# Kernel optimization log

Hardware: AMD Instinct MI355X
Metric: run time of the kernel (lower is better)

Reference implementation:

```python
import jax, jax.numpy as jnp
import numpy as np
import math

N_LEVELS = 16
F = 2
LOG2_T = 19
T = 1 << LOG2_T  # 524288 hashmap rows
BASE, FINEST = 16, 512
# b computed in float32 like torch.exp((log(512)-log(16))/15)
B_GROWTH = float(np.exp((np.log(np.float32(FINEST)) - np.log(np.float32(BASE))) / np.float32(N_LEVELS - 1)))
RES = [math.floor(BASE * B_GROWTH ** i) for i in range(N_LEVELS)]
SIZES = [(r + 1) ** 3 if r ** 3 < T else T for r in RES]
OFFS = np.concatenate([[0], np.cumsum(SIZES)]).tolist()
TOTAL_ROWS = OFFS[-1]  # 5269629
# corner order (i,j,k) for i,j,k in {0,1}, i outermost -> matches torch grid_offset
CORNER_OFF = np.array([[i, j, k] for i in (0, 1) for j in (0, 1) for k in (0, 1)], dtype=np.int32)
PRIMES = np.array([1, 2654435761, 805459861], dtype=np.uint32)
N_POINTS = 1048576


def setup_inputs() -> dict:
    key = jax.random.key(0)
    k1, k2 = jax.random.split(key)
    x = jax.random.uniform(k1, (N_POINTS, 3), dtype=jnp.float32, minval=-1.0, maxval=1.0)
    # nn.init.uniform_(-1e-4, 1e-4) on every level's embedding table
    tables = jax.random.uniform(k2, (TOTAL_ROWS, F), dtype=jnp.float32, minval=-1e-4, maxval=1e-4)
    return {"x": x, "tables": tables}


def _level_embed(x, table, res):
    # x: (B,3) in [-1,1]; table: (rows,F); res: python int (static)
    xc = jnp.clip(x, -1.0, 1.0)
    grid = jnp.float32(2.0 / res)  # (box_max-box_min)/resolution
    bl = jnp.floor((xc + 1.0) / grid).astype(jnp.int32)  # (B,3) bottom-left voxel
    vmin = bl.astype(x.dtype) * grid - 1.0               # voxel_min_vertex
    # original uses unclamped x for interpolation weights
    w = (x - vmin) / grid                                # (B,3)
    corners = bl[:, None, :] + jnp.asarray(CORNER_OFF)   # (B,8,3)
    if res ** 3 < T:
        # one-to-one hash: i*res^2 + j*res + k
        idx = corners[..., 0] * (res * res) + corners[..., 1] * res + corners[..., 2]
    else:
        # spatial hash with uint32 wraparound multiplication (matches torch int32 wrap)
        c = corners.astype(jnp.uint32)
        h = (c[..., 0] * PRIMES[0]) ^ (c[..., 1] * PRIMES[1]) ^ (c[..., 2] * PRIMES[2])
        idx = (h & jnp.uint32(T - 1)).astype(jnp.int32)
    e = table[idx]  # (B,8,F) gather
    wx, wy, wz = w[:, 0:1], w[:, 1:2], w[:, 2:3]
    c00 = e[:, 0] * (1 - wx) + e[:, 4] * wx
    c01 = e[:, 1] * (1 - wx) + e[:, 5] * wx
    c10 = e[:, 2] * (1 - wx) + e[:, 6] * wx
    c11 = e[:, 3] * (1 - wx) + e[:, 7] * wx
    c0 = c00 * (1 - wy) + c10 * wy
    c1 = c01 * (1 - wy) + c11 * wy
    return c0 * (1 - wz) + c1 * wz  # (B,F)


def reference(x, tables):
    outs = []
    for i in range(N_LEVELS):
        tab = jax.lax.slice_in_dim(tables, OFFS[i], OFFS[i + 1], axis=0)
        outs.append(_level_embed(x, tab, RES[i]))
    return jnp.concatenate(outs, axis=-1)  # (B, n_levels*F) = (B,32)
```

## Files before the change

kernel.cpp:

```cpp
#include <hip/hip_runtime.h>

#define NLVL 16
#define T_MASK ((1u << 19) - 1)
#define NBIN 32768

typedef float v2f __attribute__((ext_vector_type(2)));
typedef float v4f __attribute__((ext_vector_type(4)));

__constant__ int c_res[NLVL] = {16, 20, 25, 32, 40, 50, 64, 80,
                                101, 128, 161, 203, 256, 322, 406, 512};
__constant__ int c_off[NLVL] = {0, 4913, 14174, 31750, 67687, 136608, 269259, 543884,
                                1075325, 1599613, 2123901, 2648189, 3172477, 3696765, 4221053, 4745341};
__constant__ float c_grid[NLVL] = {
    (float)(2.0 / 16.0),  (float)(2.0 / 20.0),  (float)(2.0 / 25.0),  (float)(2.0 / 32.0),
    (float)(2.0 / 40.0),  (float)(2.0 / 50.0),  (float)(2.0 / 64.0),  (float)(2.0 / 80.0),
    (float)(2.0 / 101.0), (float)(2.0 / 128.0), (float)(2.0 / 161.0), (float)(2.0 / 203.0),
    (float)(2.0 / 256.0), (float)(2.0 / 322.0), (float)(2.0 / 406.0), (float)(2.0 / 512.0)};

constexpr int kRes[8] = {16, 20, 25, 32, 40, 50, 64, 80};
constexpr int kOff[8] = {0, 4913, 14174, 31750, 67687, 136608, 269259, 543884};
constexpr float kGrid[8] = {
    (float)(2.0 / 16.0), (float)(2.0 / 20.0), (float)(2.0 / 25.0), (float)(2.0 / 32.0),
    (float)(2.0 / 40.0), (float)(2.0 / 50.0), (float)(2.0 / 64.0), (float)(2.0 / 80.0)};

__device__ __forceinline__ void dim_setup(float xv, float grid, int& b, float& w) {
    float xc = fminf(fmaxf(xv, -1.0f), 1.0f);
    float fb = floorf((xc + 1.0f) / grid);
    b = (int)fb;
    float vmin = fb * grid - 1.0f;
    w = (xv - vmin) / grid;
}

__device__ __forceinline__ unsigned part1by2(unsigned v) {
    v &= 0x3ff;
    v = (v | (v << 16)) & 0x030000FFu;
    v = (v | (v << 8))  & 0x0300F00Fu;
    v = (v | (v << 4))  & 0x030C30C3u;
    v = (v | (v << 2))  & 0x09249249u;
    return v;
}

__device__ __forceinline__ unsigned bin3(float a, float b, float c) {
    int ba = (int)floorf((a + 1.0f) * 16.0f); ba = ba < 0 ? 0 : (ba > 31 ? 31 : ba);
    int bb = (int)floorf((b + 1.0f) * 16.0f); bb = bb < 0 ? 0 : (bb > 31 ? 31 : bb);
    int bc = (int)floorf((c + 1.0f) * 16.0f); bc = bc < 0 ? 0 : (bc > 31 ? 31 : bc);
    return part1by2((unsigned)ba) | (part1by2((unsigned)bb) << 1) | (part1by2((unsigned)bc) << 2);
}

__global__ __launch_bounds__(256) void hist_kernel(const float* __restrict__ x,
                                                   unsigned* __restrict__ hist, int n) {
    __shared__ float lx[768];
    const int p0 = (int)blockIdx.x * 256;
    const int tid = (int)threadIdx.x;
    for (int i = tid; i < 768; i += 256) {
        int gi = p0 * 3 + i;
        lx[i] = (gi < n * 3) ? x[gi] : 0.0f;
    }
    __syncthreads();
    const int p = p0 + tid;
    if (p >= n) return;
    atomicAdd(&hist[bin3(lx[3 * tid], lx[3 * tid + 1], lx[3 * tid + 2])], 1u);
}

__global__ __launch_bounds__(1024) void scan_kernel(const unsigned* __restrict__ hist,
                                                    unsigned* __restrict__ base) {
    __shared__ unsigned lh[NBIN + NBIN / 32];
    __shared__ unsigned part[1024];
    __shared__ unsigned cbase[1024];
    const int t = (int)threadIdx.x;

#pragma unroll
    for (int i = 0; i < NBIN / 1024; ++i) {
        int g = i * 1024 + t;
        lh[g + (g >> 5)] = hist[g];
    }
    __syncthreads();

    unsigned run = 0;
#pragma unroll
    for (int i = 0; i < 32; ++i) {
        unsigned v = lh[t * 33 + i];
        lh[t * 33 + i] = run;
        run += v;
    }
    part[t] = run;
    __syncthreads();

    for (int off = 1; off < 1024; off <<= 1) {
        unsigned v = (t >= off) ? part[t - off] : 0u;
        __syncthreads();
        part[t] += v;
        __syncthreads();
    }
    cbase[t] = part[t] - run;
    __syncthreads();

#pragma unroll
    for (int i = 0; i < NBIN / 1024; ++i) {
        int g = i * 1024 + t;
        base[g] = lh[g + (g >> 5)] + cbase[g >> 5];
    }
}

__global__ __launch_bounds__(256) void scatter_kernel(const float* __restrict__ x,
                                                      unsigned* __restrict__ base,
                                                      float* __restrict__ sx,
                                                      float* __restrict__ sy,
                                                      float* __restrict__ sz,
                                                      int* __restrict__ org, int n) {
    __shared__ float lx[768];
    const int p0 = (int)blockIdx.x * 256;
    const int tid = (int)threadIdx.x;
    for (int i = tid; i < 768; i += 256) {
        int gi = p0 * 3 + i;
        lx[i] = (gi < n * 3) ? x[gi] : 0.0f;
    }
    __syncthreads();
    const int p = p0 + tid;
    if (p >= n) return;
    float a = lx[3 * tid], b = lx[3 * tid + 1], c = lx[3 * tid + 2];
    unsigned slot = atomicAdd(&base[bin3(a, b, c)], 1u);
    sx[slot] = a; sy[slot] = b; sz[slot] = c; org[slot] = p;
}

__global__ __launch_bounds__(256) void gather_hash(const float* __restrict__ sx,
                                                   const float* __restrict__ sy,
                                                   const float* __restrict__ sz,
                                                   const float* __restrict__ tables,
                                                   v2f* __restrict__ ws2, int n) {
    const int level = (int)(blockIdx.x & 7) + 8;
    const int p = (int)(blockIdx.x >> 3) * 256 + (int)threadIdx.x;
    if (p >= n) return;

    const float xx = sx[p], xy = sy[p], xz = sz[p];
    const float grid = c_grid[level];
    const v2f* __restrict__ tab = reinterpret_cast<const v2f*>(tables) + c_off[level];

    int bx, by, bz;
    float wx, wy, wz;
    dim_setup(xx, grid, bx, wx);
    dim_setup(xy, grid, by, wy);
    dim_setup(xz, grid, bz, wz);

    const unsigned hx0 = (unsigned)bx, hx1 = (unsigned)(bx + 1);
    const unsigned hy0 = (unsigned)by * 2654435761u;
    const unsigned hy1 = (unsigned)(by + 1) * 2654435761u;
    const unsigned hz0 = (unsigned)bz * 805459861u;
    const unsigned hz1 = (unsigned)(bz + 1) * 805459861u;
    v2f e0 = tab[(hx0 ^ hy0 ^ hz0) & T_MASK];
    v2f e1 = tab[(hx0 ^ hy0 ^ hz1) & T_MASK];
    v2f e2 = tab[(hx0 ^ hy1 ^ hz0) & T_MASK];
    v2f e3 = tab[(hx0 ^ hy1 ^ hz1) & T_MASK];
    v2f e4 = tab[(hx1 ^ hy0 ^ hz0) & T_MASK];
    v2f e5 = tab[(hx1 ^ hy0 ^ hz1) & T_MASK];
    v2f e6 = tab[(hx1 ^ hy1 ^ hz0) & T_MASK];
    v2f e7 = tab[(hx1 ^ hy1 ^ hz1) & T_MASK];

    const float ox = 1.0f - wx, oy = 1.0f - wy, oz = 1.0f - wz;
    v2f c00 = e0 * ox + e4 * wx;
    v2f c01 = e1 * ox + e5 * wx;
    v2f c10 = e2 * ox + e6 * wx;
    v2f c11 = e3 * ox + e7 * wx;
    v2f c0 = c00 * oy + c10 * wy;
    v2f c1 = c01 * oy + c11 * wy;
    v2f r = c0 * oz + c1 * wz;

    __builtin_nontemporal_store(r, &ws2[(size_t)(level - 8) * n + p]);
}

#define ROWSTRIDE 36
__global__ __launch_bounds__(256, 4) void dense_finish(const float* __restrict__ sx,
                                                       const float* __restrict__ sy,
                                                       const float* __restrict__ sz,
                                                       const int* __restrict__ org,
                                                       const float* __restrict__ tables,
                                                       const v2f* __restrict__ ws2,
                                                       float* __restrict__ out, int n) {
    __shared__ float lrow[256 * ROWSTRIDE];
    __shared__ int lorg[256];

    const int nb = (int)gridDim.x;
    const int bid = (int)blockIdx.x;
    const int q = nb >> 3, r = nb & 7;
    const int xcd = bid & 7, j = bid >> 3;
    const int nbid = (xcd < r) ? xcd * (q + 1) + j : r * (q + 1) + (xcd - r) * q + j;
    const int tid = (int)threadIdx.x;
    const int base_p = nbid * 256;
    const int p = base_p + tid;

    if (p < n) {
        v2f h[8];
#pragma unroll
        for (int l = 0; l < 8; ++l)
            h[l] = __builtin_nontemporal_load(&ws2[(size_t)l * n + p]);

        const float xx = __builtin_nontemporal_load(&sx[p]);
        const float xy = __builtin_nontemporal_load(&sy[p]);
        const float xz = __builtin_nontemporal_load(&sz[p]);
        lorg[tid] = __builtin_nontemporal_load(&org[p]);

        v2f d[8];
#pragma unroll
        for (int l = 0; l < 8; ++l) {
            const int res = kRes[l];
            const float grid = kGrid[l];
            const v2f* __restrict__ tab = reinterpret_cast<const v2f*>(tables) + kOff[l];
            int bx, by, bz;
            float wx, wy, wz;
            dim_setup(xx, grid, bx, wx);
            dim_setup(xy, grid, by, wy);
            dim_setup(xz, grid, bz, wz);
            const int r2 = res * res;
            const int base = bx * r2 + by * res + bz;
            v2f e0 = tab[base];            v2f e1 = tab[base + 1];
            v2f e2 = tab[base + res];      v2f e3 = tab[base + res + 1];
            v2f e4 = tab[base + r2];       v2f e5 = tab[base + r2 + 1];
            v2f e6 = tab[base + r2 + res]; v2f e7 = tab[base + r2 + res + 1];
            const float ox = 1.0f - wx, oy = 1.0f - wy, oz = 1.0f - wz;
            v2f c00 = e0 * ox + e4 * wx;
            v2f c01 = e1 * ox + e5 * wx;
            v2f c10 = e2 * ox + e6 * wx;
            v2f c11 = e3 * ox + e7 * wx;
            v2f c0 = c00 * oy + c10 * wy;
            v2f c1 = c01 * oy + c11 * wy;
            d[l] = c0 * oz + c1 * wz;
        }

        float* myrow = &lrow[tid * ROWSTRIDE];
#pragma unroll
        for (int k = 0; k < 4; ++k) {
            v4f v; v.x = d[2 * k].x; v.y = d[2 * k].y; v.z = d[2 * k + 1].x; v.w = d[2 * k + 1].y;
            *reinterpret_cast<v4f*>(myrow + 4 * k) = v;
        }
#pragma unroll
        for (int k = 0; k < 4; ++k) {
            v4f v; v.x = h[2 * k].x; v.y = h[2 * k].y; v.z = h[2 * k + 1].x; v.w = h[2 * k + 1].y;
            *reinterpret_cast<v4f*>(myrow + 16 + 4 * k) = v;
        }
    }
    __syncthreads();

    const int c = tid & 7;
    const int r0 = tid >> 3;
#pragma unroll
    for (int s = 0; s < 8; ++s) {
        const int rr = s * 32 + r0;
        if (base_p + rr < n) {
            v4f v = *reinterpret_cast<const v4f*>(&lrow[rr * ROWSTRIDE + c * 4]);
            const int o = lorg[rr];
            *reinterpret_cast<v4f*>(out + (size_t)o * 32 + c * 4) = v;
        }
    }
}

__global__ __launch_bounds__(256) void hashgrid_direct(const float* __restrict__ x,
                                                       const float* __restrict__ tables,
                                                       float* __restrict__ out, int n_points) {
    const int t = (int)blockIdx.x * 256 + (int)threadIdx.x;
    const int p = t >> 4;
    if (p >= n_points) return;
    const int l = t & 15;
    const float xx = x[p * 3 + 0], xy = x[p * 3 + 1], xz = x[p * 3 + 2];
    const int res = c_res[l];
    const float grid = c_grid[l];
    const v2f* __restrict__ tab = reinterpret_cast<const v2f*>(tables) + c_off[l];
    int bx, by, bz; float wx, wy, wz;
    dim_setup(xx, grid, bx, wx);
    dim_setup(xy, grid, by, wy);
    dim_setup(xz, grid, bz, wz);
    v2f e0, e1, e2, e3, e4, e5, e6, e7;
    if (l < 8) {
        const int r2 = res * res;
        const int base = bx * r2 + by * res + bz;
        e0 = tab[base];            e1 = tab[base + 1];
        e2 = tab[base + res];      e3 = tab[base + res + 1];
        e4 = tab[base + r2];       e5 = tab[base + r2 + 1];
        e6 = tab[base + r2 + res]; e7 = tab[base + r2 + res + 1];
    } else {
        const unsigned hx0 = (unsigned)bx, hx1 = (unsigned)(bx + 1);
        const unsigned hy0 = (unsigned)by * 2654435761u, hy1 = (unsigned)(by + 1) * 2654435761u;
        const unsigned hz0 = (unsigned)bz * 805459861u,  hz1 = (unsigned)(bz + 1) * 805459861u;
        e0 = tab[(hx0 ^ hy0 ^ hz0) & T_MASK]; e1 = tab[(hx0 ^ hy0 ^ hz1) & T_MASK];
        e2 = tab[(hx0 ^ hy1 ^ hz0) & T_MASK]; e3 = tab[(hx0 ^ hy1 ^ hz1) & T_MASK];
        e4 = tab[(hx1 ^ hy0 ^ hz0) & T_MASK]; e5 = tab[(hx1 ^ hy0 ^ hz1) & T_MASK];
        e6 = tab[(hx1 ^ hy1 ^ hz0) & T_MASK]; e7 = tab[(hx1 ^ hy1 ^ hz1) & T_MASK];
    }
    const float ox = 1.0f - wx, oy = 1.0f - wy, oz = 1.0f - wz;
    v2f c00 = e0 * ox + e4 * wx, c01 = e1 * ox + e5 * wx;
    v2f c10 = e2 * ox + e6 * wx, c11 = e3 * ox + e7 * wx;
    v2f c0 = c00 * oy + c10 * wy, c1 = c01 * oy + c11 * wy;
    v2f r = c0 * oz + c1 * wz;
    reinterpret_cast<v2f*>(out)[(size_t)p * NLVL + l] = r;
}

extern "C" void kernel_launch(void* const* d_in, const int* in_sizes, int n_in,
                              void* d_out, int out_size, void* d_ws, size_t ws_size,
                              hipStream_t stream) {
    const float* x = (const float*)d_in[0];
    const float* tables = (const float*)d_in[1];
    float* out = (float*)d_out;
    const int n = in_sizes[0] / 3;

    const size_t need = 262144 + (size_t)n * 16 + (size_t)n * 64;
    if (ws_size < need) {
        const int blocks = (n * NLVL + 255) / 256;
        hipLaunchKernelGGL(hashgrid_direct, dim3(blocks), dim3(256), 0, stream, x, tables, out, n);
        return;
    }

    char* w = (char*)d_ws;
    unsigned* hist = (unsigned*)w;
    unsigned* base = (unsigned*)(w + 131072);
    float* sx = (float*)(w + 262144);
    float* sy = sx + n;
    float* sz = sy + n;
    int* org = (int*)(sz + n);
    v2f* ws2 = (v2f*)(w + 262144 + (size_t)n * 16);

    const int pb = (n + 255) / 256;

    hipMemsetAsync(hist, 0, NBIN * sizeof(unsigned), stream);
    hipLaunchKernelGGL(hist_kernel, dim3(pb), dim3(256), 0, stream, x, hist, n);
    hipLaunchKernelGGL(scan_kernel, dim3(1), dim3(1024), 0, stream, hist, base);
    hipLaunchKernelGGL(scatter_kernel, dim3(pb), dim3(256), 0, stream, x, base, sx, sy, sz, org, n);
    hipLaunchKernelGGL(gather_hash, dim3(pb * 8), dim3(256), 0, stream, sx, sy, sz, tables, ws2, n);
    hipLaunchKernelGGL(dense_finish, dim3(pb), dim3(256), 0, stream, sx, sy, sz, org, tables, ws2, out, n);
}
```

Before: 398.3 us.

## Split dense finish into separate dense-level and hash-level output store kernels

The combined finish kernel, which computed the dense levels and also reloaded the hash-level results, is split in two. One kernel computes the 8 dense levels and scatters the first 16 floats of each output row. A second kernel copies the hash-level workspace into the last 16 floats. This cuts registers and shared memory per kernel, which should raise occupancy. In exchange it adds a launch, reads the origin index twice, and writes each output row in two 64-byte halves.

```diff
diff --git a/kernel.cpp b/kernel.cpp
--- a/kernel.cpp
+++ b/kernel.cpp
@@ -168,15 +168,14 @@
     __builtin_nontemporal_store(r, &ws2[(size_t)(level - 8) * n + p]);
 }
 
-#define ROWSTRIDE 36
-__global__ __launch_bounds__(256, 4) void dense_finish(const float* __restrict__ sx,
-                                                       const float* __restrict__ sy,
-                                                       const float* __restrict__ sz,
-                                                       const int* __restrict__ org,
-                                                       const float* __restrict__ tables,
-                                                       const v2f* __restrict__ ws2,
-                                                       float* __restrict__ out, int n) {
-    __shared__ float lrow[256 * ROWSTRIDE];
+#define RS2 20
+__global__ __launch_bounds__(256, 4) void dense_store(const float* __restrict__ sx,
+                                                      const float* __restrict__ sy,
+                                                      const float* __restrict__ sz,
+                                                      const int* __restrict__ org,
+                                                      const float* __restrict__ tables,
+                                                      float* __restrict__ out, int n) {
+    __shared__ float lrow[256 * RS2];
     __shared__ int lorg[256];
 
     const int nb = (int)gridDim.x;
@@ -189,11 +188,6 @@
     const int p = base_p + tid;
 
     if (p < n) {
-        v2f h[8];
-#pragma unroll
-        for (int l = 0; l < 8; ++l)
-            h[l] = __builtin_nontemporal_load(&ws2[(size_t)l * n + p]);
-
         const float xx = __builtin_nontemporal_load(&sx[p]);
         const float xy = __builtin_nontemporal_load(&sy[p]);
         const float xz = __builtin_nontemporal_load(&sz[p]);
@@ -226,29 +220,59 @@
             d[l] = c0 * oz + c1 * wz;
         }
 
-        float* myrow = &lrow[tid * ROWSTRIDE];
+        float* myrow = &lrow[tid * RS2];
 #pragma unroll
         for (int k = 0; k < 4; ++k) {
             v4f v; v.x = d[2 * k].x; v.y = d[2 * k].y; v.z = d[2 * k + 1].x; v.w = d[2 * k + 1].y;
             *reinterpret_cast<v4f*>(myrow + 4 * k) = v;
         }
-#pragma unroll
-        for (int k = 0; k < 4; ++k) {
-            v4f v; v.x = h[2 * k].x; v.y = h[2 * k].y; v.z = h[2 * k + 1].x; v.w = h[2 * k + 1].y;
-            *reinterpret_cast<v4f*>(myrow + 16 + 4 * k) = v;
-        }
-    }
-    __syncthreads();
-
-    const int c = tid & 7;
-    const int r0 = tid >> 3;
-#pragma unroll
-    for (int s = 0; s < 8; ++s) {
-        const int rr = s * 32 + r0;
+    }
+    __syncthreads();
+
+    const int c = tid & 3;
+    const int r0 = tid >> 2;
+#pragma unroll
+    for (int s = 0; s < 4; ++s) {
+        const int rr = s * 64 + r0;
         if (base_p + rr < n) {
-            v4f v = *reinterpret_cast<const v4f*>(&lrow[rr * ROWSTRIDE + c * 4]);
+            v4f v = *reinterpret_cast<const v4f*>(&lrow[rr * RS2 + c * 4]);
             const int o = lorg[rr];
             *reinterpret_cast<v4f*>(out + (size_t)o * 32 + c * 4) = v;
+        }
+    }
+}
+
+__global__ __launch_bounds__(256) void hash_store(const v2f* __restrict__ ws2,
+                                                  const int* __restrict__ org,
+                                                  float* __restrict__ out, int n) {
+    __shared__ float lrow[256 * RS2];
+    __shared__ int lorg[256];
+    const int p0 = (int)blockIdx.x * 256;
+    const int tid = (int)threadIdx.x;
+    const int p = p0 + tid;
+
+    if (p < n) {
+        lorg[tid] = __builtin_nontemporal_load(&org[p]);
+        float* myrow = &lrow[tid * RS2];
+#pragma unroll
+        for (int l = 0; l < 4; ++l) {
+            v2f a = __builtin_nontemporal_load(&ws2[(size_t)(2 * l) * n + p]);
+            v2f b = __builtin_nontemporal_load(&ws2[(size_t)(2 * l + 1) * n + p]);
+            v4f v; v.x = a.x; v.y = a.y; v.z = b.x; v.w = b.y;
+            *reinterpret_cast<v4f*>(myrow + 4 * l) = v;
+        }
+    }
+    __syncthreads();
+
+    const int c = tid & 3;
+    const int r0 = tid >> 2;
+#pragma unroll
+    for (int s = 0; s < 4; ++s) {
+        const int rr = s * 64 + r0;
+        if (p0 + rr < n) {
+            v4f v = *reinterpret_cast<const v4f*>(&lrow[rr * RS2 + c * 4]);
+            const int o = lorg[rr];
+            *reinterpret_cast<v4f*>(out + (size_t)o * 32 + 16 + c * 4) = v;
         }
     }
 }
@@ -324,5 +348,6 @@
     hipLaunchKernelGGL(scan_kernel, dim3(1), dim3(1024), 0, stream, hist, base);
     hipLaunchKernelGGL(scatter_kernel, dim3(pb), dim3(256), 0, stream, x, base, sx, sy, sz, org, n);
     hipLaunchKernelGGL(gather_hash, dim3(pb * 8), dim3(256), 0, stream, sx, sy, sz, tables, ws2, n);
-    hipLaunchKernelGGL(dense_finish, dim3(pb), dim3(256), 0, stream, sx, sy, sz, org, tables, ws2, out, n);
-}
+    hipLaunchKernelGGL(dense_store, dim3(pb), dim3(256), 0, stream, sx, sy, sz, org, tables, out, n);
+    hipLaunchKernelGGL(hash_store, dim3(pb), dim3(256), 0, stream, ws2, org, out, n);
+}
```

New measurement: 407.8 us. +2.4%, slower.
